# Optimization experiments

Measured on AMD Instinct MI355X. Metric: run time of the kernel, lower is better.

## Reference

```python
import jax, jax.numpy as jnp
import numpy as np

N_NODES = 50000
N_EDGES = 800000
IN_CH, HID_CH, OUT_CH = 128, 256, 128


def setup_inputs() -> dict:
    key = jax.random.key(0)
    k1, k2, k3, k4 = jax.random.split(key, 4)
    x = jax.random.normal(k1, (N_NODES, IN_CH), dtype=jnp.float32)
    edge_index = jax.random.randint(k2, (2, N_EDGES), 0, N_NODES, dtype=jnp.int32)
    # Glorot-ish scaled weights
    W1 = jax.random.normal(k3, (IN_CH, HID_CH), dtype=jnp.float32) * (1.0 / np.sqrt(IN_CH))
    b1 = jnp.zeros((HID_CH,), dtype=jnp.float32)
    W2 = jax.random.normal(k4, (HID_CH, OUT_CH), dtype=jnp.float32) * (1.0 / np.sqrt(HID_CH))
    b2 = jnpp = jnp.zeros((OUT_CH,), dtype=jnp.float32)
    return {"x": x, "edge_index": edge_index, "W1": W1, "b1": b1, "W2": W2, "b2": b2}


def _gcn_conv(x, W, b, src, dst, num_nodes):
    """PyG GCNConv: add self-loops, symmetric deg^-1/2 norm, linear, scatter-add."""
    h = x @ W  # [N, out] dense transform first (as in GCNConv)
    # in-degree including self-loops (edge weights = 1)
    deg = jax.ops.segment_sum(jnp.ones_like(dst, dtype=h.dtype), dst, num_segments=num_nodes)
    deg = deg + 1.0  # self-loop contribution
    dinv = jnp.where(deg > 0, jax.lax.rsqrt(deg), 0.0)
    # neighbor messages: norm_e * h[src_e], scatter-added to dst
    norm = dinv[src] * dinv[dst]                      # [E]
    msg = h[src] * norm[:, None]                      # [E, out] gather
    agg = jax.ops.segment_sum(msg, dst, num_segments=num_nodes)  # scatter-add
    # self-loop messages: dinv[i]^2 * h[i]
    agg = agg + h * (dinv * dinv)[:, None]
    return agg + b


def reference(x, edge_index, W1, b1, W2, b2):
    src, dst = edge_index[0], edge_index[1]
    n = x.shape[0]
    h = jax.nn.relu(_gcn_conv(x, W1, b1, src, dst, n))
    return _gcn_conv(h, W2, b2, src, dst, n)
```

## Files before the change

kernel.cpp:

```cpp
#include <hip/hip_runtime.h>

#define N_NODES 50000
#define N_EDGES 800000
#define IN_CH 128
#define HID_CH 256
#define OUT_CH 128
#define BUCKET 64

using half8 = __attribute__((ext_vector_type(8))) _Float16;
using f32x4 = __attribute__((ext_vector_type(4))) float;


#define NB 391
#define NPB 128
#define BIN_CAP 2432
#define A_CHUNK 2048
#define A_BLOCKS 391

#define CVT_BLOCKS 3125
#define WT1_BLOCKS 256
#define WT2_BLOCKS 128

__global__ __launch_bounds__(256) void prepA_kernel(const int* __restrict__ src,
                                                    const int* __restrict__ dst,
                                                    int* __restrict__ bin_fill,
                                                    unsigned int* __restrict__ binbuf,
                                                    const float* __restrict__ x,
                                                    _Float16* __restrict__ x16,
                                                    const float* __restrict__ W1,
                                                    _Float16* __restrict__ W1T,
                                                    const float* __restrict__ W2,
                                                    _Float16* __restrict__ W2T) {
    __shared__ int hist[NB];
    __shared__ int lbase[NB];
    __shared__ int cur[NB];
    int b = blockIdx.x, t = threadIdx.x;
    if (b < A_BLOCKS) {
        for (int i = t; i < NB; i += 256) {
            hist[i] = 0;
            cur[i] = 0;
        }
        __syncthreads();
        int e0 = b * A_CHUNK;
        int d[8];
#pragma unroll
        for (int k = 0; k < 8; k++) {
            int i = e0 + k * 256 + t;
            d[k] = (i < N_EDGES) ? dst[i] : -1;
            if (d[k] >= 0) atomicAdd(&hist[d[k] >> 7], 1);
        }
        __syncthreads();
        for (int i = t; i < NB; i += 256)
            if (hist[i]) lbase[i] = atomicAdd(&bin_fill[i], hist[i]);
        __syncthreads();
#pragma unroll
        for (int k = 0; k < 8; k++) {
            int i = e0 + k * 256 + t;
            if (d[k] >= 0) {
                int bin = d[k] >> 7;
                int s = src[i];
                int o = atomicAdd(&cur[bin], 1);
                int pos = lbase[bin] + o;
                if (pos < BIN_CAP)
                    binbuf[(size_t)bin * BIN_CAP + pos] =
                        (unsigned)s | ((unsigned)(d[k] & (NPB - 1)) << 16);
            }
        }
    } else if (b < A_BLOCKS + CVT_BLOCKS) {
        int i = (b - A_BLOCKS) * 256 + t;
        float4 v0 = ((const float4*)x)[i * 2];
        float4 v1 = ((const float4*)x)[i * 2 + 1];
        half8 o = {(_Float16)v0.x, (_Float16)v0.y, (_Float16)v0.z, (_Float16)v0.w,
                   (_Float16)v1.x, (_Float16)v1.y, (_Float16)v1.z, (_Float16)v1.w};
        ((half8*)x16)[i] = o;
    } else if (b < A_BLOCKS + CVT_BLOCKS + WT1_BLOCKS) {
        int n = b - A_BLOCKS - CVT_BLOCKS;
        if (t < IN_CH) W1T[(size_t)n * IN_CH + t] = (_Float16)W1[(size_t)t * HID_CH + n];
    } else {
        int n = b - A_BLOCKS - CVT_BLOCKS - WT1_BLOCKS;
        if (t < HID_CH) W2T[(size_t)n * HID_CH + t] = (_Float16)W2[(size_t)t * OUT_CH + n];
    }
}

__global__ __launch_bounds__(256) void prepB_kernel(const int* __restrict__ bin_fill,
                                                    const unsigned int* __restrict__ binbuf,
                                                    int* __restrict__ cnt,
                                                    unsigned short* __restrict__ bucket) {
    __shared__ int lcnt[NPB];
    int bin = blockIdx.x, t = threadIdx.x;
    if (t < NPB) lcnt[t] = 0;
    __syncthreads();
    int n = min(bin_fill[bin], BIN_CAP);
    for (int i = t; i < n; i += 256) {
        unsigned e = binbuf[(size_t)bin * BIN_CAP + i];
        int dl = e >> 16;
        int s = e & 0xFFFF;
        int p = atomicAdd(&lcnt[dl], 1);
        if (p < BUCKET) bucket[((size_t)(bin * NPB + dl)) * BUCKET + p] = (unsigned short)s;
    }
    __syncthreads();
    int v = bin * NPB + t;
    if (t < NPB && v < N_NODES) cnt[v] = lcnt[t];
}


template <bool OUT16>
__global__ __launch_bounds__(256) void agg16_kernel(const _Float16* __restrict__ h16,
                                                    const int* __restrict__ cnt,
                                                    const unsigned short* __restrict__ bucket,
                                                    const float* __restrict__ bias,
                                                    void* __restrict__ outp) {
    int t = blockIdx.x * 256 + threadIdx.x;
    int v = t >> 4;
    int sub = t & 15;
    int deg = min(cnt[v], BUCKET);
    float dv = rsqrtf((float)cnt[v] + 1.0f);
    half8 hv = ((const half8*)(h16 + (size_t)v * 128))[sub];
    float acc[8];
#pragma unroll
    for (int i = 0; i < 8; i++) acc[i] = (float)hv[i] * dv * dv;

    const unsigned short* bk = bucket + (size_t)v * BUCKET;
    for (int base = 0; base < deg; base += 16) {
        int idx = base + sub;
        int a = 0;
        float c = 0.f;
        if (idx < deg) {
            a = bk[idx];
            c = rsqrtf((float)cnt[a] + 1.0f) * dv;
        }
        int len = min(deg - base, 16);
        int j = 0;
        for (; j + 8 <= len; j += 8) {
            int   s0 = __shfl(a, j + 0, 16); float w0 = __shfl(c, j + 0, 16);
            int   s1 = __shfl(a, j + 1, 16); float w1 = __shfl(c, j + 1, 16);
            int   s2 = __shfl(a, j + 2, 16); float w2 = __shfl(c, j + 2, 16);
            int   s3 = __shfl(a, j + 3, 16); float w3 = __shfl(c, j + 3, 16);
            int   s4 = __shfl(a, j + 4, 16); float w4 = __shfl(c, j + 4, 16);
            int   s5 = __shfl(a, j + 5, 16); float w5 = __shfl(c, j + 5, 16);
            int   s6 = __shfl(a, j + 6, 16); float w6 = __shfl(c, j + 6, 16);
            int   s7 = __shfl(a, j + 7, 16); float w7 = __shfl(c, j + 7, 16);
            half8 x0 = ((const half8*)(h16 + (size_t)s0 * 128))[sub];
            half8 x1 = ((const half8*)(h16 + (size_t)s1 * 128))[sub];
            half8 x2 = ((const half8*)(h16 + (size_t)s2 * 128))[sub];
            half8 x3 = ((const half8*)(h16 + (size_t)s3 * 128))[sub];
            half8 x4 = ((const half8*)(h16 + (size_t)s4 * 128))[sub];
            half8 x5 = ((const half8*)(h16 + (size_t)s5 * 128))[sub];
            half8 x6 = ((const half8*)(h16 + (size_t)s6 * 128))[sub];
            half8 x7 = ((const half8*)(h16 + (size_t)s7 * 128))[sub];
#pragma unroll
            for (int i = 0; i < 8; i++) acc[i] += w0 * (float)x0[i];
#pragma unroll
            for (int i = 0; i < 8; i++) acc[i] += w1 * (float)x1[i];
#pragma unroll
            for (int i = 0; i < 8; i++) acc[i] += w2 * (float)x2[i];
#pragma unroll
            for (int i = 0; i < 8; i++) acc[i] += w3 * (float)x3[i];
#pragma unroll
            for (int i = 0; i < 8; i++) acc[i] += w4 * (float)x4[i];
#pragma unroll
            for (int i = 0; i < 8; i++) acc[i] += w5 * (float)x5[i];
#pragma unroll
            for (int i = 0; i < 8; i++) acc[i] += w6 * (float)x6[i];
#pragma unroll
            for (int i = 0; i < 8; i++) acc[i] += w7 * (float)x7[i];
        }
        for (; j + 4 <= len; j += 4) {
            int   s0 = __shfl(a, j + 0, 16); float w0 = __shfl(c, j + 0, 16);
            int   s1 = __shfl(a, j + 1, 16); float w1 = __shfl(c, j + 1, 16);
            int   s2 = __shfl(a, j + 2, 16); float w2 = __shfl(c, j + 2, 16);
            int   s3 = __shfl(a, j + 3, 16); float w3 = __shfl(c, j + 3, 16);
            half8 x0 = ((const half8*)(h16 + (size_t)s0 * 128))[sub];
            half8 x1 = ((const half8*)(h16 + (size_t)s1 * 128))[sub];
            half8 x2 = ((const half8*)(h16 + (size_t)s2 * 128))[sub];
            half8 x3 = ((const half8*)(h16 + (size_t)s3 * 128))[sub];
#pragma unroll
            for (int i = 0; i < 8; i++) acc[i] += w0 * (float)x0[i];
#pragma unroll
            for (int i = 0; i < 8; i++) acc[i] += w1 * (float)x1[i];
#pragma unroll
            for (int i = 0; i < 8; i++) acc[i] += w2 * (float)x2[i];
#pragma unroll
            for (int i = 0; i < 8; i++) acc[i] += w3 * (float)x3[i];
        }
        for (; j < len; j++) {
            int   s = __shfl(a, j, 16);
            float w = __shfl(c, j, 16);
            half8 xv = ((const half8*)(h16 + (size_t)s * 128))[sub];
#pragma unroll
            for (int i = 0; i < 8; i++) acc[i] += w * (float)xv[i];
        }
    }

    if (OUT16) {
        half8 o;
#pragma unroll
        for (int i = 0; i < 8; i++) o[i] = (_Float16)acc[i];
        ((half8*)outp)[(size_t)v * 16 + sub] = o;
    } else {
        const float4* bp = (const float4*)bias;
        float4 b0 = bp[sub * 2], b1v = bp[sub * 2 + 1];
        float4 o0 = make_float4(acc[0] + b0.x, acc[1] + b0.y, acc[2] + b0.z, acc[3] + b0.w);
        float4 o1 = make_float4(acc[4] + b1v.x, acc[5] + b1v.y, acc[6] + b1v.z, acc[7] + b1v.w);
        float4* op = (float4*)outp;
        op[(size_t)v * 32 + sub * 2] = o0;
        op[(size_t)v * 32 + sub * 2 + 1] = o1;
    }
}


__global__ __launch_bounds__(256) void fused_mlp_kernel(const _Float16* __restrict__ A,
                                                        const _Float16* __restrict__ W1T,
                                                        const float* __restrict__ b1,
                                                        const _Float16* __restrict__ W2T,
                                                        _Float16* __restrict__ T2, int M) {
    const int LDH = 264;
    const int LDA = 136;
    __shared__ __align__(16) _Float16 h1s[64 * LDH];
    __shared__ __align__(16) _Float16 As[64 * LDA];

    int tid = threadIdx.x;
    int wave = tid >> 6, lane = tid & 63;
    int quad = lane >> 4, l16 = lane & 15;
    int wm = wave >> 1, wn = wave & 1;
    int bm = blockIdx.x * 64;

    for (int q = tid; q < 64 * 16; q += 256) {
        int row = q >> 4, seg = q & 15;
        int gr = bm + row;
        float4 v = make_float4(0.f, 0.f, 0.f, 0.f);
        if (gr < M) v = *(const float4*)(A + (size_t)gr * IN_CH + seg * 8);
        *(float4*)(As + row * LDA + seg * 8) = v;
    }
    __syncthreads();

    for (int nh = 0; nh < 2; nh++) {
        f32x4 acc[2][4] = {};
#pragma unroll
        for (int k0 = 0; k0 < IN_CH; k0 += 32) {
            half8 af[2], bf[4];
#pragma unroll
            for (int nt = 0; nt < 4; nt++)
                bf[nt] = *(const half8*)(W1T + (size_t)(nh * 128 + wn * 64 + nt * 16 + l16) * IN_CH +
                                         k0 + quad * 8);
#pragma unroll
            for (int mt = 0; mt < 2; mt++)
                af[mt] = *(const half8*)(As + (wm * 32 + mt * 16 + l16) * LDA + k0 + quad * 8);
#pragma unroll
            for (int mt = 0; mt < 2; mt++)
#pragma unroll
                for (int nt = 0; nt < 4; nt++)
                    acc[mt][nt] = __builtin_amdgcn_mfma_f32_16x16x32_f16(af[mt], bf[nt], acc[mt][nt], 0, 0, 0);
        }
#pragma unroll
        for (int mt = 0; mt < 2; mt++)
#pragma unroll
            for (int nt = 0; nt < 4; nt++)
#pragma unroll
                for (int r = 0; r < 4; r++) {
                    int ml = wm * 32 + mt * 16 + quad * 4 + r;
                    int nl = wn * 64 + nt * 16 + l16;
                    float v = acc[mt][nt][r] + b1[nh * 128 + nl];
                    h1s[ml * LDH + nh * 128 + nl] = (_Float16)fmaxf(v, 0.f);
                }
    }
    __syncthreads();

    f32x4 acc2[2][4] = {};
#pragma unroll 4
    for (int k0 = 0; k0 < HID_CH; k0 += 32) {
        half8 af[2], bf[4];
#pragma unroll
        for (int nt = 0; nt < 4; nt++)
            bf[nt] = *(const half8*)(W2T + (size_t)(wn * 64 + nt * 16 + l16) * HID_CH + k0 + quad * 8);
#pragma unroll
        for (int mt = 0; mt < 2; mt++)
            af[mt] = *(const half8*)(h1s + (wm * 32 + mt * 16 + l16) * LDH + k0 + quad * 8);
#pragma unroll
        for (int mt = 0; mt < 2; mt++)
#pragma unroll
            for (int nt = 0; nt < 4; nt++)
                acc2[mt][nt] = __builtin_amdgcn_mfma_f32_16x16x32_f16(af[mt], bf[nt], acc2[mt][nt], 0, 0, 0);
    }

    _Float16* Cs = As;
#pragma unroll
    for (int mt = 0; mt < 2; mt++)
#pragma unroll
        for (int nt = 0; nt < 4; nt++)
#pragma unroll
            for (int r = 0; r < 4; r++) {
                int ml = wm * 32 + mt * 16 + quad * 4 + r;
                int nl = wn * 64 + nt * 16 + l16;
                Cs[ml * LDA + nl] = (_Float16)acc2[mt][nt][r];
            }
    __syncthreads();
    for (int q = tid; q < 64 * 16; q += 256) {
        int row = q >> 4, seg = q & 15;
        int gr = bm + row;
        if (gr < M)
            *(float4*)(T2 + (size_t)gr * OUT_CH + seg * 8) = *(const float4*)(Cs + row * LDA + seg * 8);
    }
}


extern "C" void kernel_launch(void* const* d_in, const int* in_sizes, int n_in,
                              void* d_out, int out_size, void* d_ws, size_t ws_size,
                              hipStream_t stream) {
    const float* x  = (const float*)d_in[0];
    const int*   ei = (const int*)d_in[1];
    const int*   src = ei;
    const int*   dst = ei + N_EDGES;
    const float* W1 = (const float*)d_in[2];
    const float* b1 = (const float*)d_in[3];
    const float* W2 = (const float*)d_in[4];
    const float* b2 = (const float*)d_in[5];
    float* out = (float*)d_out;

    char* w = (char*)d_ws;
    auto alloc = [&](size_t bytes) -> void* {
        void* p = (void*)w;
        w += (bytes + 255) & ~(size_t)255;
        return p;
    };
    int*            cnt     = (int*)alloc((size_t)N_NODES * 4);
    unsigned short* bucket  = (unsigned short*)alloc((size_t)N_NODES * BUCKET * 2);
    _Float16*       x16     = (_Float16*)alloc((size_t)N_NODES * IN_CH * 2);
    _Float16*       a1      = (_Float16*)alloc((size_t)N_NODES * IN_CH * 2);
    _Float16*       t2      = (_Float16*)alloc((size_t)N_NODES * OUT_CH * 2);
    _Float16*       W1T     = (_Float16*)alloc((size_t)IN_CH * HID_CH * 2);
    _Float16*       W2T     = (_Float16*)alloc((size_t)HID_CH * OUT_CH * 2);
    int*            bin_fill = (int*)alloc((size_t)NB * 4);
    unsigned int*   binbuf   = (unsigned int*)alloc((size_t)NB * BIN_CAP * 4);

    hipMemsetAsync(bin_fill, 0, (size_t)NB * 4, stream);

    prepA_kernel<<<A_BLOCKS + CVT_BLOCKS + WT1_BLOCKS + WT2_BLOCKS, 256, 0, stream>>>(
        src, dst, bin_fill, binbuf, x, x16, W1, W1T, W2, W2T);
    prepB_kernel<<<NB, 256, 0, stream>>>(bin_fill, binbuf, cnt, bucket);

    agg16_kernel<true><<<N_NODES * 16 / 256, 256, 0, stream>>>(x16, cnt, bucket, nullptr, a1);
    fused_mlp_kernel<<<(N_NODES + 63) / 64, 256, 0, stream>>>(a1, W1T, b1, W2T, t2, N_NODES);
    agg16_kernel<false><<<N_NODES * 16 / 256, 256, 0, stream>>>(t2, cnt, bucket, b2, out);
}
```

Baseline: 211.0 us.

## Stage buckets in LDS, pad aggregation to 8-wide groups, double prepA chunk

```diff
diff --git a/kernel.cpp b/kernel.cpp
--- a/kernel.cpp
+++ b/kernel.cpp
@@ -14,8 +14,8 @@
 #define NB 391
 #define NPB 128
 #define BIN_CAP 2432
-#define A_CHUNK 2048
-#define A_BLOCKS 391
+#define A_CHUNK 4096
+#define A_BLOCKS 196
 
 #define CVT_BLOCKS 3125
 #define WT1_BLOCKS 256
@@ -42,9 +42,9 @@
         }
         __syncthreads();
         int e0 = b * A_CHUNK;
-        int d[8];
-#pragma unroll
-        for (int k = 0; k < 8; k++) {
+        int d[16];
+#pragma unroll
+        for (int k = 0; k < 16; k++) {
             int i = e0 + k * 256 + t;
             d[k] = (i < N_EDGES) ? dst[i] : -1;
             if (d[k] >= 0) atomicAdd(&hist[d[k] >> 7], 1);
@@ -54,7 +54,7 @@
             if (hist[i]) lbase[i] = atomicAdd(&bin_fill[i], hist[i]);
         __syncthreads();
 #pragma unroll
-        for (int k = 0; k < 8; k++) {
+        for (int k = 0; k < 16; k++) {
             int i = e0 + k * 256 + t;
             if (d[k] >= 0) {
                 int bin = d[k] >> 7;
@@ -87,6 +87,7 @@
                                                     int* __restrict__ cnt,
                                                     unsigned short* __restrict__ bucket) {
     __shared__ int lcnt[NPB];
+    __shared__ __align__(16) unsigned short lbk[NPB][BUCKET];
     int bin = blockIdx.x, t = threadIdx.x;
     if (t < NPB) lcnt[t] = 0;
     __syncthreads();
@@ -96,9 +97,15 @@
         int dl = e >> 16;
         int s = e & 0xFFFF;
         int p = atomicAdd(&lcnt[dl], 1);
-        if (p < BUCKET) bucket[((size_t)(bin * NPB + dl)) * BUCKET + p] = (unsigned short)s;
-    }
-    __syncthreads();
+        if (p < BUCKET) lbk[dl][p] = (unsigned short)s;
+    }
+    __syncthreads();
+    const uint4* lp = (const uint4*)lbk;
+    uint4* gp = (uint4*)(bucket + (size_t)bin * NPB * BUCKET);
+    for (int q = t; q < NPB * BUCKET / 8; q += 256) {
+        int row = q >> 3;
+        if (bin * NPB + row < N_NODES) gp[q] = lp[q];
+    }
     int v = bin * NPB + t;
     if (t < NPB && v < N_NODES) cnt[v] = lcnt[t];
 }
@@ -113,84 +120,53 @@
     int t = blockIdx.x * 256 + threadIdx.x;
     int v = t >> 4;
     int sub = t & 15;
-    int deg = min(cnt[v], BUCKET);
-    float dv = rsqrtf((float)cnt[v] + 1.0f);
+    int degr = cnt[v];
+    int deg = min(degr, BUCKET);
+    float dv = rsqrtf((float)degr + 1.0f);
     half8 hv = ((const half8*)(h16 + (size_t)v * 128))[sub];
     float acc[8];
 #pragma unroll
     for (int i = 0; i < 8; i++) acc[i] = (float)hv[i] * dv * dv;
+
+#define PROCESS8(J)                                                                   \
+    {                                                                                 \
+        int   s0 = __shfl(a, (J) + 0, 16); float w0 = __shfl(c, (J) + 0, 16);         \
+        int   s1 = __shfl(a, (J) + 1, 16); float w1 = __shfl(c, (J) + 1, 16);         \
+        int   s2 = __shfl(a, (J) + 2, 16); float w2 = __shfl(c, (J) + 2, 16);         \
+        int   s3 = __shfl(a, (J) + 3, 16); float w3 = __shfl(c, (J) + 3, 16);         \
+        int   s4 = __shfl(a, (J) + 4, 16); float w4 = __shfl(c, (J) + 4, 16);         \
+        int   s5 = __shfl(a, (J) + 5, 16); float w5 = __shfl(c, (J) + 5, 16);         \
+        int   s6 = __shfl(a, (J) + 6, 16); float w6 = __shfl(c, (J) + 6, 16);         \
+        int   s7 = __shfl(a, (J) + 7, 16); float w7 = __shfl(c, (J) + 7, 16);         \
+        half8 x0 = ((const half8*)(h16 + (size_t)s0 * 128))[sub];                     \
+        half8 x1 = ((const half8*)(h16 + (size_t)s1 * 128))[sub];                     \
+        half8 x2 = ((const half8*)(h16 + (size_t)s2 * 128))[sub];                     \
+        half8 x3 = ((const half8*)(h16 + (size_t)s3 * 128))[sub];                     \
+        half8 x4 = ((const half8*)(h16 + (size_t)s4 * 128))[sub];                     \
+        half8 x5 = ((const half8*)(h16 + (size_t)s5 * 128))[sub];                     \
+        half8 x6 = ((const half8*)(h16 + (size_t)s6 * 128))[sub];                     \
+        half8 x7 = ((const half8*)(h16 + (size_t)s7 * 128))[sub];                     \
+        _Pragma("unroll") for (int i = 0; i < 8; i++) acc[i] += w0 * (float)x0[i];    \
+        _Pragma("unroll") for (int i = 0; i < 8; i++) acc[i] += w1 * (float)x1[i];    \
+        _Pragma("unroll") for (int i = 0; i < 8; i++) acc[i] += w2 * (float)x2[i];    \
+        _Pragma("unroll") for (int i = 0; i < 8; i++) acc[i] += w3 * (float)x3[i];    \
+        _Pragma("unroll") for (int i = 0; i < 8; i++) acc[i] += w4 * (float)x4[i];    \
+        _Pragma("unroll") for (int i = 0; i < 8; i++) acc[i] += w5 * (float)x5[i];    \
+        _Pragma("unroll") for (int i = 0; i < 8; i++) acc[i] += w6 * (float)x6[i];    \
+        _Pragma("unroll") for (int i = 0; i < 8; i++) acc[i] += w7 * (float)x7[i];    \
+    }
 
     const unsigned short* bk = bucket + (size_t)v * BUCKET;
     for (int base = 0; base < deg; base += 16) {
         int idx = base + sub;
-        int a = 0;
-        float c = 0.f;
-        if (idx < deg) {
-            a = bk[idx];
-            c = rsqrtf((float)cnt[a] + 1.0f) * dv;
-        }
-        int len = min(deg - base, 16);
-        int j = 0;
-        for (; j + 8 <= len; j += 8) {
-            int   s0 = __shfl(a, j + 0, 16); float w0 = __shfl(c, j + 0, 16);
-            int   s1 = __shfl(a, j + 1, 16); float w1 = __shfl(c, j + 1, 16);
-            int   s2 = __shfl(a, j + 2, 16); float w2 = __shfl(c, j + 2, 16);
-            int   s3 = __shfl(a, j + 3, 16); float w3 = __shfl(c, j + 3, 16);
-            int   s4 = __shfl(a, j + 4, 16); float w4 = __shfl(c, j + 4, 16);
-            int   s5 = __shfl(a, j + 5, 16); float w5 = __shfl(c, j + 5, 16);
-            int   s6 = __shfl(a, j + 6, 16); float w6 = __shfl(c, j + 6, 16);
-            int   s7 = __shfl(a, j + 7, 16); float w7 = __shfl(c, j + 7, 16);
-            half8 x0 = ((const half8*)(h16 + (size_t)s0 * 128))[sub];
-            half8 x1 = ((const half8*)(h16 + (size_t)s1 * 128))[sub];
-            half8 x2 = ((const half8*)(h16 + (size_t)s2 * 128))[sub];
-            half8 x3 = ((const half8*)(h16 + (size_t)s3 * 128))[sub];
-            half8 x4 = ((const half8*)(h16 + (size_t)s4 * 128))[sub];
-            half8 x5 = ((const half8*)(h16 + (size_t)s5 * 128))[sub];
-            half8 x6 = ((const half8*)(h16 + (size_t)s6 * 128))[sub];
-            half8 x7 = ((const half8*)(h16 + (size_t)s7 * 128))[sub];
-#pragma unroll
-            for (int i = 0; i < 8; i++) acc[i] += w0 * (float)x0[i];
-#pragma unroll
-            for (int i = 0; i < 8; i++) acc[i] += w1 * (float)x1[i];
-#pragma unroll
-            for (int i = 0; i < 8; i++) acc[i] += w2 * (float)x2[i];
-#pragma unroll
-            for (int i = 0; i < 8; i++) acc[i] += w3 * (float)x3[i];
-#pragma unroll
-            for (int i = 0; i < 8; i++) acc[i] += w4 * (float)x4[i];
-#pragma unroll
-            for (int i = 0; i < 8; i++) acc[i] += w5 * (float)x5[i];
-#pragma unroll
-            for (int i = 0; i < 8; i++) acc[i] += w6 * (float)x6[i];
-#pragma unroll
-            for (int i = 0; i < 8; i++) acc[i] += w7 * (float)x7[i];
-        }
-        for (; j + 4 <= len; j += 4) {
-            int   s0 = __shfl(a, j + 0, 16); float w0 = __shfl(c, j + 0, 16);
-            int   s1 = __shfl(a, j + 1, 16); float w1 = __shfl(c, j + 1, 16);
-            int   s2 = __shfl(a, j + 2, 16); float w2 = __shfl(c, j + 2, 16);
-            int   s3 = __shfl(a, j + 3, 16); float w3 = __shfl(c, j + 3, 16);
-            half8 x0 = ((const half8*)(h16 + (size_t)s0 * 128))[sub];
-            half8 x1 = ((const half8*)(h16 + (size_t)s1 * 128))[sub];
-            half8 x2 = ((const half8*)(h16 + (size_t)s2 * 128))[sub];
-            half8 x3 = ((const half8*)(h16 + (size_t)s3 * 128))[sub];
-#pragma unroll
-            for (int i = 0; i < 8; i++) acc[i] += w0 * (float)x0[i];
-#pragma unroll
-            for (int i = 0; i < 8; i++) acc[i] += w1 * (float)x1[i];
-#pragma unroll
-            for (int i = 0; i < 8; i++) acc[i] += w2 * (float)x2[i];
-#pragma unroll
-            for (int i = 0; i < 8; i++) acc[i] += w3 * (float)x3[i];
-        }
-        for (; j < len; j++) {
-            int   s = __shfl(a, j, 16);
-            float w = __shfl(c, j, 16);
-            half8 xv = ((const half8*)(h16 + (size_t)s * 128))[sub];
-#pragma unroll
-            for (int i = 0; i < 8; i++) acc[i] += w * (float)xv[i];
-        }
-    }
+        int am = (int)bk[min(idx, BUCKET - 1)];
+        bool ok = idx < deg;
+        int a = ok ? am : 0;
+        float c = ok ? rsqrtf((float)cnt[a] + 1.0f) * dv : 0.f;
+        PROCESS8(0)
+        if (base + 8 < deg) PROCESS8(8)
+    }
+#undef PROCESS8
 
     if (OUT16) {
         half8 o;
```

Measured after the change: 206.1 us. 2.3% less time.
